# Performance work log

Measured on AMD Instinct MI355X. Metric: run time of the kernel, lower is better.

The kernel has to match this reference:

```python
import jax, jax.numpy as jnp
import numpy as np

N = 2097152

def _net(x, W1, b1, W2, b2, W3, b3):
    # Net: 4 -> 64 -> 64 -> 1 MLP with ReLU
    h = jax.nn.relu(x @ W1 + b1)
    h = jax.nn.relu(h @ W2 + b2)
    return h @ W3 + b3  # [..., 1]

def setup_inputs() -> dict:
    key = jax.random.key(0)
    ks = jax.random.split(key, 7)
    def init_w(k, fan_in, fan_out):
        return (jax.random.normal(k, (fan_in, fan_out), jnp.float32)
                * np.float32(np.sqrt(2.0 / fan_in)))
    return {
        "states": jax.random.normal(ks[0], (N, 4), jnp.float32),
        "W1": init_w(ks[1], 4, 64),
        "b1": jnp.zeros((64,), jnp.float32),
        "W2": init_w(ks[2], 64, 64),
        "b2": jnp.zeros((64,), jnp.float32),
        "W3": init_w(ks[3], 64, 1),
        "b3": jnp.zeros((1,), jnp.float32),
    }

def reference(states, W1, b1, W2, b2, W3, b3):
    # log Q(s) = net(s) - log(sum_i exp(net(e_i))) ; loss = -sum_s log Q(s)
    logits = _net(states, W1, b1, W2, b2, W3, b3)            # [N, 1]
    denom_logits = _net(jnp.eye(4, dtype=states.dtype),       # 4 one-hot states
                        W1, b1, W2, b2, W3, b3)               # [4, 1]
    log_denom = jax.nn.logsumexp(denom_logits)                # scalar
    n = jnp.asarray(states.shape[0], states.dtype)
    loss = -(jnp.sum(logits) - n * log_denom)
    return loss.reshape(1)  # original accumulates shape-[1] tensors
```

## Files before the change

kernel.cpp:

```cpp
#include <hip/hip_runtime.h>
#include <hip/hip_bf16.h>

typedef __bf16 bf16x8 __attribute__((ext_vector_type(8)));
typedef float  f32x4  __attribute__((ext_vector_type(4)));

#define MAIN_BLOCKS 2048

__global__ __launch_bounds__(256) void qloss_main(
    const float* __restrict__ states, const float* __restrict__ W1,
    const float* __restrict__ b1, const float* __restrict__ W2,
    const float* __restrict__ b2, const float* __restrict__ W3,
    int n_states, double* __restrict__ partials)
{
    const int lane = threadIdx.x & 63;
    const int wave = threadIdx.x >> 6;
    const int g = lane >> 4;
    const int r = lane & 15;

    float w1r[4][16], b1r[16];
#pragma unroll
    for (int j = 0; j < 16; ++j) {
        const int k = 8*g + (j & 7) + 32*(j >> 3);
        b1r[j] = b1[k];
#pragma unroll
        for (int i = 0; i < 4; ++i) w1r[i][j] = W1[i*64 + k];
    }

    bf16x8 w2f[4][2];
#pragma unroll
    for (int t = 0; t < 4; ++t)
#pragma unroll
        for (int ks = 0; ks < 2; ++ks)
#pragma unroll
            for (int e = 0; e < 8; ++e) {
                const int k = 8*g + e + 32*ks;
                w2f[t][ks][e] = (__bf16)W2[k*64 + (r + 16*t)];
            }

    float b2r[4], w3r[4];
#pragma unroll
    for (int t = 0; t < 4; ++t) { b2r[t] = b2[r + 16*t]; w3r[t] = W3[r + 16*t]; }

    const int ntiles = n_states >> 4;
    const int waves_per_blk = blockDim.x >> 6;
    const int nwaves = gridDim.x * waves_per_blk;
    const float4* __restrict__ st4 = (const float4*)states;

    float psum = 0.f;
    for (int tile = blockIdx.x * waves_per_blk + wave; tile < ntiles; tile += nwaves) {
        const float4 x = st4[tile*16 + r];

        bf16x8 af[2];
#pragma unroll
        for (int ks = 0; ks < 2; ++ks)
#pragma unroll
            for (int e = 0; e < 8; ++e) {
                const int j = ks*8 + e;
                float t = fmaf(x.x, w1r[0][j], b1r[j]);
                t = fmaf(x.y, w1r[1][j], t);
                t = fmaf(x.z, w1r[2][j], t);
                t = fmaf(x.w, w1r[3][j], t);
                af[ks][e] = (__bf16)fmaxf(t, 0.f);
            }

#pragma unroll
        for (int t4 = 0; t4 < 4; ++t4) {
            f32x4 acc = { b2r[t4], b2r[t4], b2r[t4], b2r[t4] };
            acc = __builtin_amdgcn_mfma_f32_16x16x32_bf16(af[0], w2f[t4][0], acc, 0, 0, 0);
            acc = __builtin_amdgcn_mfma_f32_16x16x32_bf16(af[1], w2f[t4][1], acc, 0, 0, 0);
#pragma unroll
            for (int rr = 0; rr < 4; ++rr)
                psum = fmaf(fmaxf(acc[rr], 0.f), w3r[t4], psum);
        }
    }

#pragma unroll
    for (int off = 32; off; off >>= 1) psum += __shfl_xor(psum, off, 64);
    __shared__ float wpart[4];
    if (lane == 0) wpart[wave] = psum;
    __syncthreads();
    if (threadIdx.x == 0)
        partials[blockIdx.x] = (double)(wpart[0] + wpart[1] + wpart[2] + wpart[3]);
}

__global__ __launch_bounds__(256) void qloss_finalize(
    const float* __restrict__ W1, const float* __restrict__ b1,
    const float* __restrict__ W2, const float* __restrict__ b2,
    const float* __restrict__ W3, const float* __restrict__ b3,
    const double* __restrict__ partials, int nparts,
    int n_states, float* __restrict__ out)
{
    const int lane = threadIdx.x & 63;
    const int wave = threadIdx.x >> 6;

    __shared__ float  dlog[4];
    __shared__ double wsum[4];

    float h1 = fmaxf(W1[wave*64 + lane] + b1[lane], 0.f);
    float acc = b2[lane];
    for (int k = 0; k < 64; ++k)
        acc = fmaf(__shfl(h1, k, 64), W2[k*64 + lane], acc);
    float c = fmaxf(acc, 0.f) * W3[lane];
#pragma unroll
    for (int off = 32; off; off >>= 1) c += __shfl_xor(c, off, 64);
    if (lane == 0) dlog[wave] = c + b3[0];

    double ps = 0.0;
    for (int i = threadIdx.x; i < nparts; i += blockDim.x) ps += partials[i];
#pragma unroll
    for (int off = 32; off; off >>= 1) ps += __shfl_xor(ps, off, 64);
    if (lane == 0) wsum[wave] = ps;

    __syncthreads();
    if (threadIdx.x == 0) {
        const double S = wsum[0] + wsum[1] + wsum[2] + wsum[3];
        double m = dlog[0];
        for (int i = 1; i < 4; ++i) m = fmax(m, (double)dlog[i]);
        double e = 0.0;
        for (int i = 0; i < 4; ++i) e += exp((double)dlog[i] - m);
        const double lse = m + log(e);
        const double nn = (double)n_states;
        const double logits_sum = S + nn * (double)b3[0];
        out[0] = (float)(-(logits_sum - nn * lse));
    }
}

extern "C" void kernel_launch(void* const* d_in, const int* in_sizes, int n_in,
                              void* d_out, int out_size, void* d_ws, size_t ws_size,
                              hipStream_t stream)
{
    const float* states = (const float*)d_in[0];
    const float* W1 = (const float*)d_in[1];
    const float* b1 = (const float*)d_in[2];
    const float* W2 = (const float*)d_in[3];
    const float* b2 = (const float*)d_in[4];
    const float* W3 = (const float*)d_in[5];
    const float* b3 = (const float*)d_in[6];
    float* out = (float*)d_out;

    const int n_states = in_sizes[0] / 4;

    int nb = MAIN_BLOCKS;
    const size_t max_parts = ws_size / sizeof(double);
    if ((size_t)nb > max_parts) nb = (int)max_parts;
    if (nb < 1) nb = 1;
    double* partials = (double*)d_ws;

    qloss_main<<<nb, 256, 0, stream>>>(states, W1, b1, W2, b2, W3, n_states, partials);
    qloss_finalize<<<1, 256, 0, stream>>>(W1, b1, W2, b2, W3, b3, partials, nb, n_states, out);
}
```

Measured before the change: 51.01 us.

## Use fp16 dot2 for first layer and prefetch next tile's states

```diff
diff --git a/kernel.cpp b/kernel.cpp
--- a/kernel.cpp
+++ b/kernel.cpp
@@ -1,12 +1,24 @@
 #include <hip/hip_runtime.h>
 #include <hip/hip_bf16.h>
+#include <hip/hip_fp16.h>
 
 typedef __bf16 bf16x8 __attribute__((ext_vector_type(8)));
 typedef float  f32x4  __attribute__((ext_vector_type(4)));
+typedef _Float16 h2   __attribute__((ext_vector_type(2)));
 
 #define MAIN_BLOCKS 2048
 
-__global__ __launch_bounds__(256) void qloss_main(
+#if defined(__has_builtin)
+#  if __has_builtin(__builtin_amdgcn_fdot2)
+#    define HAVE_FDOT2 1
+#  else
+#    define HAVE_FDOT2 0
+#  endif
+#else
+#  define HAVE_FDOT2 0
+#endif
+
+__global__ __launch_bounds__(256, 1) void qloss_main(
     const float* __restrict__ states, const float* __restrict__ W1,
     const float* __restrict__ b1, const float* __restrict__ W2,
     const float* __restrict__ b2, const float* __restrict__ W3,
@@ -17,13 +29,23 @@
     const int g = lane >> 4;
     const int r = lane & 15;
 
-    float w1r[4][16], b1r[16];
+    float b1r[16];
+#if HAVE_FDOT2
+    h2 w1p[2][16];
+#else
+    float w1r[4][16];
+#endif
 #pragma unroll
     for (int j = 0; j < 16; ++j) {
         const int k = 8*g + (j & 7) + 32*(j >> 3);
         b1r[j] = b1[k];
+#if HAVE_FDOT2
+        w1p[0][j] = h2{(_Float16)W1[0*64 + k], (_Float16)W1[1*64 + k]};
+        w1p[1][j] = h2{(_Float16)W1[2*64 + k], (_Float16)W1[3*64 + k]};
+#else
 #pragma unroll
         for (int i = 0; i < 4; ++i) w1r[i][j] = W1[i*64 + k];
+#endif
     }
 
     bf16x8 w2f[4][2];
@@ -47,19 +69,34 @@
     const float4* __restrict__ st4 = (const float4*)states;
 
     float psum = 0.f;
-    for (int tile = blockIdx.x * waves_per_blk + wave; tile < ntiles; tile += nwaves) {
-        const float4 x = st4[tile*16 + r];
+    const int tile0 = blockIdx.x * waves_per_blk + wave;
+    float4 xc = {0.f, 0.f, 0.f, 0.f};
+    if (tile0 < ntiles) xc = st4[tile0*16 + r];
 
+    for (int tile = tile0; tile < ntiles; tile += nwaves) {
+        const int nxt = tile + nwaves;
+        const int nidx = (nxt < ntiles) ? nxt : tile;
+        const float4 xn = st4[nidx*16 + r];
+
+#if HAVE_FDOT2
+        const h2 x01 = {(_Float16)xc.x, (_Float16)xc.y};
+        const h2 x23 = {(_Float16)xc.z, (_Float16)xc.w};
+#endif
         bf16x8 af[2];
 #pragma unroll
         for (int ks = 0; ks < 2; ++ks)
 #pragma unroll
             for (int e = 0; e < 8; ++e) {
                 const int j = ks*8 + e;
-                float t = fmaf(x.x, w1r[0][j], b1r[j]);
-                t = fmaf(x.y, w1r[1][j], t);
-                t = fmaf(x.z, w1r[2][j], t);
-                t = fmaf(x.w, w1r[3][j], t);
+#if HAVE_FDOT2
+                float t = __builtin_amdgcn_fdot2(x01, w1p[0][j], b1r[j], false);
+                t       = __builtin_amdgcn_fdot2(x23, w1p[1][j], t, false);
+#else
+                float t = fmaf(xc.x, w1r[0][j], b1r[j]);
+                t = fmaf(xc.y, w1r[1][j], t);
+                t = fmaf(xc.z, w1r[2][j], t);
+                t = fmaf(xc.w, w1r[3][j], t);
+#endif
                 af[ks][e] = (__bf16)fmaxf(t, 0.f);
             }
 
@@ -72,6 +109,8 @@
             for (int rr = 0; rr < 4; ++rr)
                 psum = fmaf(fmaxf(acc[rr], 0.f), w3r[t4], psum);
         }
+
+        xc = xn;
     }
 
 #pragma unroll
```

After: 53.84 us. 1.06x slower.

## Use fp16 dot2 for layer one, packed bf16 convert, and prefetch states

Applied to the files above, without the earlier changes.

```diff
diff --git a/kernel.cpp b/kernel.cpp
--- a/kernel.cpp
+++ b/kernel.cpp
@@ -1,10 +1,14 @@
 #include <hip/hip_runtime.h>
 #include <hip/hip_bf16.h>
+#include <hip/hip_fp16.h>
+#include <stdint.h>
 
 typedef __bf16 bf16x8 __attribute__((ext_vector_type(8)));
 typedef float  f32x4  __attribute__((ext_vector_type(4)));
+typedef _Float16 h2   __attribute__((ext_vector_type(2)));
+typedef int    i32x4  __attribute__((ext_vector_type(4)));
 
-#define MAIN_BLOCKS 2048
+#define MAIN_BLOCKS 1024
 
 __global__ __launch_bounds__(256) void qloss_main(
     const float* __restrict__ states, const float* __restrict__ W1,
@@ -17,13 +21,14 @@
     const int g = lane >> 4;
     const int r = lane & 15;
 
-    float w1r[4][16], b1r[16];
+    float b1r[16];
+    h2 w1p[2][16];
 #pragma unroll
     for (int j = 0; j < 16; ++j) {
         const int k = 8*g + (j & 7) + 32*(j >> 3);
         b1r[j] = b1[k];
-#pragma unroll
-        for (int i = 0; i < 4; ++i) w1r[i][j] = W1[i*64 + k];
+        w1p[0][j] = h2{(_Float16)W1[0*64 + k], (_Float16)W1[1*64 + k]};
+        w1p[1][j] = h2{(_Float16)W1[2*64 + k], (_Float16)W1[3*64 + k]};
     }
 
     bf16x8 w2f[4][2];
@@ -41,39 +46,69 @@
 #pragma unroll
     for (int t = 0; t < 4; ++t) { b2r[t] = b2[r + 16*t]; w3r[t] = W3[r + 16*t]; }
 
+#pragma unroll
+    for (int j = 0; j < 16; ++j) {
+        asm("" : "+v"(b1r[j]));
+        asm("" : "+v"(w1p[0][j]), "+v"(w1p[1][j]));
+    }
+#pragma unroll
+    for (int t = 0; t < 4; ++t) {
+        asm("" : "+v"(w2f[t][0]), "+v"(w2f[t][1]));
+        asm("" : "+v"(b2r[t]), "+v"(w3r[t]));
+    }
+
     const int ntiles = n_states >> 4;
     const int waves_per_blk = blockDim.x >> 6;
     const int nwaves = gridDim.x * waves_per_blk;
     const float4* __restrict__ st4 = (const float4*)states;
 
-    float psum = 0.f;
-    for (int tile = blockIdx.x * waves_per_blk + wave; tile < ntiles; tile += nwaves) {
-        const float4 x = st4[tile*16 + r];
+    float ps0 = 0.f, ps1 = 0.f;
+    const int tile0 = blockIdx.x * waves_per_blk + wave;
+    float4 xc = {0.f, 0.f, 0.f, 0.f};
+    if (tile0 < ntiles) xc = st4[tile0*16 + r];
 
-        bf16x8 af[2];
+    for (int tile = tile0; tile < ntiles; tile += nwaves) {
+        const int nxt = tile + nwaves;
+        const int nidx = (nxt < ntiles) ? nxt : tile;
+        const float4 xn = st4[nidx*16 + r];
+
+        const h2 x01 = {(_Float16)xc.x, (_Float16)xc.y};
+        const h2 x23 = {(_Float16)xc.z, (_Float16)xc.w};
+        i32x4 aw0, aw1;
 #pragma unroll
-        for (int ks = 0; ks < 2; ++ks)
+        for (int ks = 0; ks < 2; ++ks) {
 #pragma unroll
-            for (int e = 0; e < 8; ++e) {
-                const int j = ks*8 + e;
-                float t = fmaf(x.x, w1r[0][j], b1r[j]);
-                t = fmaf(x.y, w1r[1][j], t);
-                t = fmaf(x.z, w1r[2][j], t);
-                t = fmaf(x.w, w1r[3][j], t);
-                af[ks][e] = (__bf16)fmaxf(t, 0.f);
+            for (int w = 0; w < 4; ++w) {
+                const int j0 = ks*8 + 2*w, j1 = j0 + 1;
+                float t0 = __builtin_amdgcn_fdot2(x01, w1p[0][j0], b1r[j0], false);
+                t0       = __builtin_amdgcn_fdot2(x23, w1p[1][j0], t0, false);
+                float t1 = __builtin_amdgcn_fdot2(x01, w1p[0][j1], b1r[j1], false);
+                t1       = __builtin_amdgcn_fdot2(x23, w1p[1][j1], t1, false);
+                t0 = fmaxf(t0, 0.f);
+                t1 = fmaxf(t1, 0.f);
+                int w32;
+                asm("v_cvt_pk_bf16_f32 %0, %1, %2" : "=v"(w32) : "v"(t0), "v"(t1));
+                if (ks == 0) aw0[w] = w32; else aw1[w] = w32;
             }
+        }
+        const bf16x8 af0 = __builtin_bit_cast(bf16x8, aw0);
+        const bf16x8 af1 = __builtin_bit_cast(bf16x8, aw1);
 
 #pragma unroll
         for (int t4 = 0; t4 < 4; ++t4) {
             f32x4 acc = { b2r[t4], b2r[t4], b2r[t4], b2r[t4] };
-            acc = __builtin_amdgcn_mfma_f32_16x16x32_bf16(af[0], w2f[t4][0], acc, 0, 0, 0);
-            acc = __builtin_amdgcn_mfma_f32_16x16x32_bf16(af[1], w2f[t4][1], acc, 0, 0, 0);
-#pragma unroll
-            for (int rr = 0; rr < 4; ++rr)
-                psum = fmaf(fmaxf(acc[rr], 0.f), w3r[t4], psum);
+            acc = __builtin_amdgcn_mfma_f32_16x16x32_bf16(af0, w2f[t4][0], acc, 0, 0, 0);
+            acc = __builtin_amdgcn_mfma_f32_16x16x32_bf16(af1, w2f[t4][1], acc, 0, 0, 0);
+            ps0 = fmaf(fmaxf(acc[0], 0.f), w3r[t4], ps0);
+            ps1 = fmaf(fmaxf(acc[1], 0.f), w3r[t4], ps1);
+            ps0 = fmaf(fmaxf(acc[2], 0.f), w3r[t4], ps0);
+            ps1 = fmaf(fmaxf(acc[3], 0.f), w3r[t4], ps1);
         }
+
+        xc = xn;
     }
 
+    float psum = ps0 + ps1;
 #pragma unroll
     for (int off = 32; off; off >>= 1) psum += __shfl_xor(psum, off, 64);
     __shared__ float wpart[4];
```

After: 52.93 us. +3.8%, slower.
